# Performance work log

Hardware: AMD Instinct MI355X
Metric: run time of the kernel (lower is better)

## Reference

```python
import jax, jax.numpy as jnp
import numpy as np

B, S, HID = 4, 1024, 1024
NH, HD = 16, 64  # num heads, head dim


def setup_inputs() -> dict:
    key = jax.random.key(0)
    ks = jax.random.split(key, 8)
    scale = 0.02
    return {
        "hidden_states": jax.random.normal(ks[0], (B, S, HID), dtype=jnp.float32),
        "attention_mask": jnp.ones((B, 1, 1, S), dtype=jnp.float32),
        "Wq": jax.random.normal(ks[1], (HID, HID), dtype=jnp.float32) * scale,
        "bq": jnp.zeros((HID,), dtype=jnp.float32),
        "Wk": jax.random.normal(ks[2], (HID, HID), dtype=jnp.float32) * scale,
        "bk": jnp.zeros((HID,), dtype=jnp.float32),
        "Wv": jax.random.normal(ks[3], (HID, HID), dtype=jnp.float32) * scale,
        "bv": jnp.zeros((HID,), dtype=jnp.float32),
    }


def reference(hidden_states, attention_mask, Wq, bq, Wk, bk, Wv, bv):
    # Linear projections: torch nn.Linear computes x @ W.T + b
    q = hidden_states @ Wq.T + bq  # [B,S,HID]
    k = hidden_states @ Wk.T + bk
    v = hidden_states @ Wv.T + bv

    def split_heads(x):
        return x.reshape(B, S, NH, HD).transpose(0, 2, 1, 3)  # [B,NH,S,HD]

    q, k, v = split_heads(q), split_heads(k), split_heads(v)

    scores = jnp.einsum("bhqd,bhkd->bhqk", q, k) / jnp.sqrt(jnp.float32(HD))
    # faithful to original: scores - (2 - mask) * 1e6
    scores = scores - (2.0 - attention_mask) * 1.0e6
    probs = jax.nn.softmax(scores, axis=-1)
    # dropout: eval mode -> identity
    ctx = jnp.einsum("bhqk,bhkd->bhqd", probs, v)  # [B,NH,S,HD]
    ctx = ctx.transpose(0, 2, 1, 3).reshape(B, S, HID)
    return ctx
```

## Files before the change

kernel.cpp:

```cpp
#include <hip/hip_runtime.h>
#include <math.h>

#define B_ 4
#define S_ 1024
#define HID_ 1024
#define NH_ 16
#define HD_ 64
#define NTOK (B_ * S_)

typedef __attribute__((ext_vector_type(4))) float f32x4;
typedef __attribute__((ext_vector_type(8))) short bf16x8;

__device__ __forceinline__ unsigned short f2bf(float f) {
    union { float f; unsigned int u; } v; v.f = f;
    unsigned int r = v.u + 0x7fffu + ((v.u >> 16) & 1u);
    return (unsigned short)(r >> 16);
}

#if __has_builtin(__builtin_amdgcn_cvt_pk_bf16_f32)
__device__ __forceinline__ unsigned int pk_bf16(float a, float b) {
    auto v = __builtin_amdgcn_cvt_pk_bf16_f32(a, b);
    union { decltype(v) v; unsigned int u; } cv; cv.v = v;
    return cv.u;
}
#else
__device__ __forceinline__ unsigned int pk_bf16(float a, float b) {
    return (unsigned int)f2bf(a) | ((unsigned int)f2bf(b) << 16);
}
#endif

__device__ __forceinline__ void load_lds16(const void* g, void* l) {
    __builtin_amdgcn_global_load_lds(
        (const __attribute__((address_space(1))) unsigned int*)(uintptr_t)g,
        (__attribute__((address_space(3))) unsigned int*)(uintptr_t)l,
        16, 0, 0);
}

__global__ __launch_bounds__(256) void cvt_all(
    const float* __restrict__ x, const float* __restrict__ wq,
    const float* __restrict__ wk, const float* __restrict__ wv,
    unsigned short* __restrict__ xb, unsigned short* __restrict__ wqb,
    unsigned short* __restrict__ wkb, unsigned short* __restrict__ wvb)
{
    const int which = blockIdx.y;
    const float* src = which == 0 ? x : which == 1 ? wq : which == 2 ? wk : wv;
    unsigned short* dst = which == 0 ? xb : which == 1 ? wqb : which == 2 ? wkb : wvb;
    const int n4 = (which == 0) ? (NTOK * HID_ / 4) : (HID_ * HID_ / 4);
    int i = blockIdx.x * 256 + threadIdx.x;
    if (i < n4) {
        float4 f = ((const float4*)src)[i];
        uint2 o;
        o.x = pk_bf16(f.x, f.y);
        o.y = pk_bf16(f.z, f.w);
        ((uint2*)dst)[i] = o;
    }
}

__global__ __launch_bounds__(512, 6) void qkv_gemm_mfma(
    const unsigned short* __restrict__ xb,
    const unsigned short* __restrict__ Wqb, const float* __restrict__ bq,
    const unsigned short* __restrict__ Wkb, const float* __restrict__ bk,
    const unsigned short* __restrict__ Wvb, const float* __restrict__ bv,
    unsigned short* __restrict__ qout, unsigned short* __restrict__ kout,
    unsigned short* __restrict__ vtout)
{
    const int which = blockIdx.z;
    const unsigned short* __restrict__ W = which == 0 ? Wqb : which == 1 ? Wkb : Wvb;
    const float* __restrict__ bias       = which == 0 ? bq  : which == 1 ? bk  : bv;

    __shared__ unsigned short As[128 * 64];
    __shared__ unsigned short Bs[128 * 64];

    const int t    = threadIdx.x;
    const int lane = t & 63;
    const int w    = t >> 6;
    const int wr   = w >> 2;
    const int wc   = w & 3;
    const int g    = lane >> 4;
    const int lrow = lane & 15;

    const int bm = blockIdx.x;
    const int bn = blockIdx.y;

    const unsigned short* __restrict__ Arow = (which == 2) ? W  : xb;
    const unsigned short* __restrict__ Brow = (which == 2) ? xb : W;
    const int am0 = (which == 2) ? bn * 128 : bm * 128;
    const int bn0 = (which == 2) ? bm * 128 : bn * 128;

    const int srow = t >> 3;
    const int sc   = ((t & 7) ^ ((t >> 3) & 7)) << 3;
    const unsigned short* gA = Arow + (size_t)(am0 + srow) * HID_ + sc;
    const unsigned short* gB = Brow + (size_t)(bn0 + srow) * HID_ + sc;

    const f32x4 zero = {0.f, 0.f, 0.f, 0.f};
    f32x4 acc[4][2];
    #pragma unroll
    for (int i = 0; i < 4; ++i)
        #pragma unroll
        for (int j = 0; j < 2; ++j) acc[i][j] = zero;

    for (int k0 = 0; k0 < HID_; k0 += 64) {
        __syncthreads();
        #pragma unroll
        for (int i = 0; i < 2; ++i) {
            load_lds16(gA + (size_t)(i * 64) * HID_ + k0, (char*)As + i * 8192 + t * 16);
            load_lds16(gB + (size_t)(i * 64) * HID_ + k0, (char*)Bs + i * 8192 + t * 16);
        }
        __syncthreads();

        #pragma unroll
        for (int ks = 0; ks < 2; ++ks) {
            bf16x8 af[4], bf[2];
            #pragma unroll
            for (int i = 0; i < 4; ++i) {
                const int row = wr * 64 + i * 16 + lrow;
                af[i] = *(const bf16x8*)&As[row * 64 + (((ks * 4 + g) ^ (row & 7)) << 3)];
            }
            #pragma unroll
            for (int j = 0; j < 2; ++j) {
                const int row = wc * 32 + j * 16 + lrow;
                bf[j] = *(const bf16x8*)&Bs[row * 64 + (((ks * 4 + g) ^ (row & 7)) << 3)];
            }
            #pragma unroll
            for (int i = 0; i < 4; ++i)
                #pragma unroll
                for (int j = 0; j < 2; ++j)
                    acc[i][j] = __builtin_amdgcn_mfma_f32_16x16x32_bf16(
                        af[i], bf[j], acc[i][j], 0, 0, 0);
        }
    }

    const int col   = lane & 15;
    const int rbase = (lane >> 4) << 2;
    if (which == 2) {
        #pragma unroll
        for (int i = 0; i < 4; ++i) {
            #pragma unroll
            for (int r = 0; r < 4; ++r) {
                const int feat = bn * 128 + wr * 64 + i * 16 + rbase + r;
                const int h = feat >> 6, d = feat & 63;
                const float bias_v = bias[feat];
                #pragma unroll
                for (int j = 0; j < 2; ++j) {
                    const int tok = bm * 128 + wc * 32 + j * 16 + col;
                    const int b = tok >> 10, s = tok & 1023;
                    vtout[((size_t)((b << 4) + h) << 16) + ((size_t)d << 10) + s] =
                        f2bf(acc[i][j][r] + bias_v);
                }
            }
        }
    } else {
        #pragma unroll
        for (int j = 0; j < 2; ++j) {
            const int feat = bn * 128 + wc * 32 + j * 16 + col;
            const int h = feat >> 6, d = feat & 63;
            const float bias_v = bias[feat];
            #pragma unroll
            for (int i = 0; i < 4; ++i) {
                const int tok0 = bm * 128 + wr * 64 + i * 16 + rbase;
                #pragma unroll
                for (int r = 0; r < 4; ++r) {
                    const int tok = tok0 + r;
                    const int b = tok >> 10, s = tok & 1023;
                    const size_t off = ((size_t)((b << 4) + h) << 16) + ((size_t)s << 6) + d;
                    const float val = acc[i][j][r] + bias_v;
                    if (which == 0) qout[off] = f2bf(val);
                    else            kout[off] = f2bf(val);
                }
            }
        }
    }
}

__global__ __launch_bounds__(512, 4) void attn_mfma(
    const unsigned short* __restrict__ Q, const unsigned short* __restrict__ K,
    const unsigned short* __restrict__ Vt, const float* __restrict__ mask,
    float* __restrict__ out)
{
    __shared__ unsigned short Qs[128 * 64];
    __shared__ unsigned short Ks[64 * 64];
    __shared__ unsigned short Vts[64 * 64];
    __shared__ unsigned short Ps[8][16 * 72];
    __shared__ float Ls[8][16];
    __shared__ float Ms[64];

    const int t    = threadIdx.x;
    const int lane = t & 63;
    const int w    = t >> 6;
    const int g    = lane >> 4;
    const int ln   = lane & 15;

    const int bh = blockIdx.x;
    const int b  = bh >> 4;
    const int h  = bh & 15;
    const int q0 = blockIdx.y << 7;

    const unsigned short* __restrict__ qg = Q  + ((size_t)bh << 16);
    const unsigned short* __restrict__ kg = K  + ((size_t)bh << 16);
    const unsigned short* __restrict__ vg = Vt + ((size_t)bh << 16);

    #pragma unroll
    for (int i = 0; i < 2; ++i) {
        const int G   = i * 512 + t;
        const int row = G >> 3;
        const int c   = (G & 7) ^ (row & 7);
        load_lds16(qg + (size_t)(q0 + row) * 64 + c * 8, (char*)Qs + i * 8192 + t * 16);
    }

    const f32x4 zero = {0.f, 0.f, 0.f, 0.f};
    f32x4 O[4];
    #pragma unroll
    for (int j = 0; j < 4; ++j) O[j] = zero;
    float lacc = 0.f;

    const int qrow = w * 16 + ln;

    for (int kt = 0; kt < 16; ++kt) {
        const int kt0 = kt << 6;
        __syncthreads();
        {
            const int row = t >> 3;
            const int c   = (t & 7) ^ (row & 7);
            load_lds16(kg + (size_t)(kt0 + row) * 64 + c * 8, (char*)Ks  + t * 16);
            load_lds16(vg + (size_t)row * 1024 + kt0 + c * 8, (char*)Vts + t * 16);
        }
        if (t < 64) Ms[t] = mask[(b << 10) + kt0 + t];
        __syncthreads();

        f32x4 sacc[4];
        #pragma unroll
        for (int j = 0; j < 4; ++j) sacc[j] = zero;
        #pragma unroll
        for (int ks = 0; ks < 2; ++ks) {
            bf16x8 qf = *(const bf16x8*)&Qs[qrow * 64 + (((ks * 4 + g) ^ (qrow & 7)) << 3)];
            bf16x8 kf[4];
            #pragma unroll
            for (int j = 0; j < 4; ++j) {
                const int krow = j * 16 + ln;
                kf[j] = *(const bf16x8*)&Ks[krow * 64 + (((ks * 4 + g) ^ (krow & 7)) << 3)];
            }
            #pragma unroll
            for (int j = 0; j < 4; ++j)
                sacc[j] = __builtin_amdgcn_mfma_f32_16x16x32_bf16(
                    kf[j], qf, sacc[j], 0, 0, 0);
        }

        #pragma unroll
        for (int j = 0; j < 4; ++j) {
            float p[4];
            #pragma unroll
            for (int r = 0; r < 4; ++r) {
                const int key = j * 16 + g * 4 + r;
                const float sv = sacc[j][r] * 0.125f - (2.0f - Ms[key]) * 1.0e6f;
                p[r] = __expf(sv + 1.0e6f);
            }
            lacc += (p[0] + p[1]) + (p[2] + p[3]);
            uint2 pk;
            pk.x = pk_bf16(p[0], p[1]);
            pk.y = pk_bf16(p[2], p[3]);
            *(uint2*)&Ps[w][ln * 72 + j * 16 + (g << 2)] = pk;
        }
        asm volatile("s_waitcnt lgkmcnt(0)" ::: "memory");

        #pragma unroll
        for (int ks = 0; ks < 2; ++ks) {
            bf16x8 pf = *(const bf16x8*)&Ps[w][ln * 72 + ks * 32 + (g << 3)];
            bf16x8 vf[4];
            #pragma unroll
            for (int j = 0; j < 4; ++j) {
                const int vrow = j * 16 + ln;
                vf[j] = *(const bf16x8*)&Vts[vrow * 64 + (((ks * 4 + g) ^ (vrow & 7)) << 3)];
            }
            #pragma unroll
            for (int j = 0; j < 4; ++j)
                O[j] = __builtin_amdgcn_mfma_f32_16x16x32_bf16(
                    pf, vf[j], O[j], 0, 0, 0);
        }
    }

    float rs = lacc;
    rs += __shfl_xor(rs, 16);
    rs += __shfl_xor(rs, 32);
    if (lane < 16) Ls[w][ln] = rs;
    asm volatile("s_waitcnt lgkmcnt(0)" ::: "memory");
    #pragma unroll
    for (int r = 0; r < 4; ++r) {
        const float inv = 1.0f / Ls[w][(g << 2) + r];
        const int q = q0 + w * 16 + (g << 2) + r;
        const size_t base = (((size_t)(b << 10) + q) << 10) + (h << 6);
        #pragma unroll
        for (int j = 0; j < 4; ++j)
            out[base + j * 16 + ln] = O[j][r] * inv;
    }
}

extern "C" void kernel_launch(void* const* d_in, const int* in_sizes, int n_in,
                              void* d_out, int out_size, void* d_ws, size_t ws_size,
                              hipStream_t stream) {
    const float* hs   = (const float*)d_in[0];
    const float* mask = (const float*)d_in[1];
    const float* Wq   = (const float*)d_in[2];
    const float* bq   = (const float*)d_in[3];
    const float* Wk   = (const float*)d_in[4];
    const float* bk   = (const float*)d_in[5];
    const float* Wv   = (const float*)d_in[6];
    const float* bv   = (const float*)d_in[7];
    float* out = (float*)d_out;

    char* ws = (char*)d_ws;
    unsigned short* xb  = (unsigned short*)(ws);
    unsigned short* wqb = (unsigned short*)(ws + ((size_t)8  << 20));
    unsigned short* wkb = (unsigned short*)(ws + ((size_t)10 << 20));
    unsigned short* wvb = (unsigned short*)(ws + ((size_t)12 << 20));
    unsigned short* qb  = (unsigned short*)(ws + ((size_t)14 << 20));
    unsigned short* kb  = (unsigned short*)(ws + ((size_t)22 << 20));
    unsigned short* vtb = (unsigned short*)(ws + ((size_t)30 << 20));

    cvt_all<<<dim3(4096, 4), 256, 0, stream>>>(hs, Wq, Wk, Wv, xb, wqb, wkb, wvb);
    qkv_gemm_mfma<<<dim3(NTOK / 128, HID_ / 128, 3), 512, 0, stream>>>(
        xb, wqb, bq, wkb, bk, wvb, bv, qb, kb, vtb);
    attn_mfma<<<dim3(B_ * NH_, S_ / 128), 512, 0, stream>>>(qb, kb, vtb, mask, out);
}
```

Measured before the change: 154.6 us.

## Keep Q fragments in registers and process 128-key tiles per barrier pair

Q fragments now load straight from global memory into registers instead of being staged through LDS. Each outer iteration stages two 64-key K/V sub-tiles, so the loop runs 8 iterations instead of 16. This halves the number of block-wide barriers and cuts the LDS reads of Q on every tile. The cost is a few more registers and the same total LDS use, since the Q buffer is swapped for a second K/V buffer, which could affect occupancy at the 4-block launch bound.

```diff
diff --git a/kernel.cpp b/kernel.cpp
--- a/kernel.cpp
+++ b/kernel.cpp
@@ -177,12 +177,11 @@
     const unsigned short* __restrict__ Vt, const float* __restrict__ mask,
     float* __restrict__ out)
 {
-    __shared__ unsigned short Qs[128 * 64];
-    __shared__ unsigned short Ks[64 * 64];
-    __shared__ unsigned short Vts[64 * 64];
+    __shared__ unsigned short Ks[2][64 * 64];
+    __shared__ unsigned short Vts[2][64 * 64];
     __shared__ unsigned short Ps[8][16 * 72];
     __shared__ float Ls[8][16];
-    __shared__ float Ms[64];
+    __shared__ float Ms2[128];
 
     const int t    = threadIdx.x;
     const int lane = t & 63;
@@ -199,13 +198,12 @@
     const unsigned short* __restrict__ kg = K  + ((size_t)bh << 16);
     const unsigned short* __restrict__ vg = Vt + ((size_t)bh << 16);
 
+    const int qrow = w * 16 + ln;
+
+    bf16x8 qreg[2];
     #pragma unroll
-    for (int i = 0; i < 2; ++i) {
-        const int G   = i * 512 + t;
-        const int row = G >> 3;
-        const int c   = (G & 7) ^ (row & 7);
-        load_lds16(qg + (size_t)(q0 + row) * 64 + c * 8, (char*)Qs + i * 8192 + t * 16);
-    }
+    for (int ks = 0; ks < 2; ++ks)
+        qreg[ks] = *(const bf16x8*)&qg[(size_t)(q0 + qrow) * 64 + ks * 32 + (g << 3)];
 
     const f32x4 zero = {0.f, 0.f, 0.f, 0.f};
     f32x4 O[4];
@@ -213,68 +211,72 @@
     for (int j = 0; j < 4; ++j) O[j] = zero;
     float lacc = 0.f;
 
-    const int qrow = w * 16 + ln;
-
-    for (int kt = 0; kt < 16; ++kt) {
-        const int kt0 = kt << 6;
+    for (int kt2 = 0; kt2 < 8; ++kt2) {
+        const int kt0 = kt2 << 7;
         __syncthreads();
         {
             const int row = t >> 3;
             const int c   = (t & 7) ^ (row & 7);
-            load_lds16(kg + (size_t)(kt0 + row) * 64 + c * 8, (char*)Ks  + t * 16);
-            load_lds16(vg + (size_t)row * 1024 + kt0 + c * 8, (char*)Vts + t * 16);
-        }
-        if (t < 64) Ms[t] = mask[(b << 10) + kt0 + t];
+            #pragma unroll
+            for (int s = 0; s < 2; ++s) {
+                const int kb0 = kt0 + (s << 6);
+                load_lds16(kg + (size_t)(kb0 + row) * 64 + c * 8, (char*)Ks[s]  + t * 16);
+                load_lds16(vg + (size_t)row * 1024 + kb0 + c * 8, (char*)Vts[s] + t * 16);
+            }
+        }
+        if (t < 128) Ms2[t] = mask[(b << 10) + kt0 + t];
         __syncthreads();
 
-        f32x4 sacc[4];
-        #pragma unroll
-        for (int j = 0; j < 4; ++j) sacc[j] = zero;
-        #pragma unroll
-        for (int ks = 0; ks < 2; ++ks) {
-            bf16x8 qf = *(const bf16x8*)&Qs[qrow * 64 + (((ks * 4 + g) ^ (qrow & 7)) << 3)];
-            bf16x8 kf[4];
+        #pragma unroll
+        for (int s = 0; s < 2; ++s) {
+            f32x4 sacc[4];
+            #pragma unroll
+            for (int j = 0; j < 4; ++j) sacc[j] = zero;
+            #pragma unroll
+            for (int ks = 0; ks < 2; ++ks) {
+                bf16x8 kf[4];
+                #pragma unroll
+                for (int j = 0; j < 4; ++j) {
+                    const int krow = j * 16 + ln;
+                    kf[j] = *(const bf16x8*)&Ks[s][krow * 64 + (((ks * 4 + g) ^ (krow & 7)) << 3)];
+                }
+                #pragma unroll
+                for (int j = 0; j < 4; ++j)
+                    sacc[j] = __builtin_amdgcn_mfma_f32_16x16x32_bf16(
+                        kf[j], qreg[ks], sacc[j], 0, 0, 0);
+            }
+
             #pragma unroll
             for (int j = 0; j < 4; ++j) {
-                const int krow = j * 16 + ln;
-                kf[j] = *(const bf16x8*)&Ks[krow * 64 + (((ks * 4 + g) ^ (krow & 7)) << 3)];
-            }
-            #pragma unroll
-            for (int j = 0; j < 4; ++j)
-                sacc[j] = __builtin_amdgcn_mfma_f32_16x16x32_bf16(
-                    kf[j], qf, sacc[j], 0, 0, 0);
-        }
-
-        #pragma unroll
-        for (int j = 0; j < 4; ++j) {
-            float p[4];
-            #pragma unroll
-            for (int r = 0; r < 4; ++r) {
-                const int key = j * 16 + g * 4 + r;
-                const float sv = sacc[j][r] * 0.125f - (2.0f - Ms[key]) * 1.0e6f;
-                p[r] = __expf(sv + 1.0e6f);
-            }
-            lacc += (p[0] + p[1]) + (p[2] + p[3]);
-            uint2 pk;
-            pk.x = pk_bf16(p[0], p[1]);
-            pk.y = pk_bf16(p[2], p[3]);
-            *(uint2*)&Ps[w][ln * 72 + j * 16 + (g << 2)] = pk;
-        }
-        asm volatile("s_waitcnt lgkmcnt(0)" ::: "memory");
-
-        #pragma unroll
-        for (int ks = 0; ks < 2; ++ks) {
-            bf16x8 pf = *(const bf16x8*)&Ps[w][ln * 72 + ks * 32 + (g << 3)];
-            bf16x8 vf[4];
-            #pragma unroll
-            for (int j = 0; j < 4; ++j) {
-                const int vrow = j * 16 + ln;
-                vf[j] = *(const bf16x8*)&Vts[vrow * 64 + (((ks * 4 + g) ^ (vrow & 7)) << 3)];
-            }
-            #pragma unroll
-            for (int j = 0; j < 4; ++j)
-                O[j] = __builtin_amdgcn_mfma_f32_16x16x32_bf16(
-                    pf, vf[j], O[j], 0, 0, 0);
+                float p[4];
+                #pragma unroll
+                for (int r = 0; r < 4; ++r) {
+                    const int key = j * 16 + g * 4 + r;
+                    const float sv = sacc[j][r] * 0.125f - (2.0f - Ms2[(s << 6) + key]) * 1.0e6f;
+                    p[r] = __expf(sv + 1.0e6f);
+                }
+                lacc += (p[0] + p[1]) + (p[2] + p[3]);
+                uint2 pk;
+                pk.x = pk_bf16(p[0], p[1]);
+                pk.y = pk_bf16(p[2], p[3]);
+                *(uint2*)&Ps[w][ln * 72 + j * 16 + (g << 2)] = pk;
+            }
+            asm volatile("s_waitcnt lgkmcnt(0)" ::: "memory");
+
+            #pragma unroll
+            for (int ks = 0; ks < 2; ++ks) {
+                bf16x8 pf = *(const bf16x8*)&Ps[w][ln * 72 + ks * 32 + (g << 3)];
+                bf16x8 vf[4];
+                #pragma unroll
+                for (int j = 0; j < 4; ++j) {
+                    const int vrow = j * 16 + ln;
+                    vf[j] = *(const bf16x8*)&Vts[s][vrow * 64 + (((ks * 4 + g) ^ (vrow & 7)) << 3)];
+                }
+                #pragma unroll
+                for (int j = 0; j < 4; ++j)
+                    O[j] = __builtin_amdgcn_mfma_f32_16x16x32_bf16(
+                        pf, vf[j], O[j], 0, 0, 0);
+            }
         }
     }
 
```

Measured after the change: 154.6 us. No clear change (-0.0%).
